# Optimization experiments

Hardware: AMD Instinct MI355X
Metric: run time of the kernel (lower is better)

Reference implementation:

```python
import jax, jax.numpy as jnp
import numpy as np

ALPHA = 0.9     # projection strength
EPS = 1e-3      # Lyapunov positive-definite regularizer (lyapunov_eps)
B, D, H = 32768, 512, 64


def setup_inputs() -> dict:
    key = jax.random.key(0)
    ks = jax.random.split(key, 8)
    def w(k, shape, fan_in):
        return jax.random.normal(k, shape, jnp.float32) * (1.0 / fan_in) ** 0.5
    return dict(
        x=jax.random.normal(ks[0], (B, D), jnp.float32),
        # dynamics MLP f(x): D -> 64 -> 64 -> D
        W1=w(ks[1], (D, H), D), b1=jnp.zeros((H,), jnp.float32),
        W2=w(ks[2], (H, H), H), b2=jnp.zeros((H,), jnp.float32),
        W3=w(ks[3], (H, D), H), b3=jnp.zeros((D,), jnp.float32),
        # Lyapunov MLP V(z): D -> 64 -> 64 -> 1 (+ eps*||z||^2)
        V1=w(ks[4], (D, H), D), c1=jnp.zeros((H,), jnp.float32),
        V2=w(ks[5], (H, H), H), c2=jnp.zeros((H,), jnp.float32),
        V3=w(ks[6], (H, 1), H), c3=jnp.zeros((1,), jnp.float32),
    )


def reference(x, W1, b1, W2, b2, W3, b3, V1, c1, V2, c2, V3, c3):
    def fnet(xx):  # nominal dynamics: [B,D] -> [B,D]
        h = jax.nn.relu(xx @ W1 + b1)
        h = jax.nn.relu(h @ W2 + b2)
        return h @ W3 + b3

    def vnet(z):  # Lyapunov candidate: [B,D] -> [B]
        h = jax.nn.relu(z @ V1 + c1)
        h = jax.nn.relu(h @ V2 + c2)
        return (h @ V3 + c3)[..., 0] + EPS * jnp.sum(z * z, axis=-1)

    def lyap_sum(xx):
        v = vnet(fnet(xx))
        return jnp.sum(v), v

    # grad_v replicates the in-forward lyapunov.backward(...): dV(f(x))/dx, shape [B,D]
    (_, lyap), grad_v = jax.value_and_grad(lyap_sum, has_aux=True)(x)

    f = fnet(x)                                   # [B, D]
    dot = jnp.sum(grad_v * grad_v, axis=-1)       # bmm(gv, fv): per-sample <grad_v, grad_v>
    denom = jnp.sum(grad_v * grad_v)              # global .pow(2).sum() over all elements
    orth = jax.nn.relu(dot + ALPHA * lyap) / denom  # [B]
    return f - orth[:, None] * grad_v             # diag_embed(orth) @ grad_v
```

## Files before the change

### kernel.cpp

```cpp
#include <hip/hip_runtime.h>

#define ALPHA_C 0.9f
#define EPS_C 1e-3f

typedef unsigned short u16;
typedef __attribute__((ext_vector_type(8))) short short8;
typedef __attribute__((ext_vector_type(4))) float f32x4;
#define MFMA(a, b, c) __builtin_amdgcn_mfma_f32_16x16x32_bf16(a, b, c, 0, 0, 0)

__device__ __forceinline__ u16 f2bf(float f) {
  union { float f; unsigned u; } v; v.f = f;
  unsigned u = v.u;
  u += 0x7FFFu + ((u >> 16) & 1u);
  return (u16)(u >> 16);
}
__device__ __forceinline__ float bf2f(u16 h) {
  union { unsigned u; float f; } v; v.u = ((unsigned)h) << 16;
  return v.f;
}

__global__ __launch_bounds__(256) void k_conv(
    const float* __restrict__ W1, const float* __restrict__ W2, const float* __restrict__ W3,
    const float* __restrict__ V1, const float* __restrict__ V2,
    u16* __restrict__ W1T, u16* __restrict__ W1n, u16* __restrict__ W2T, u16* __restrict__ W2n,
    u16* __restrict__ W3T, u16* __restrict__ W3n, u16* __restrict__ V1T, u16* __restrict__ V1n,
    u16* __restrict__ V2T, u16* __restrict__ V2n) {
  int i = blockIdx.x * 256 + threadIdx.x;
  { float v = W1[i]; int k = i >> 6, j = i & 63; u16 b = f2bf(v); W1n[i] = b; W1T[j * 512 + k] = b; }
  { float v = V1[i]; int k = i >> 6, j = i & 63; u16 b = f2bf(v); V1n[i] = b; V1T[j * 512 + k] = b; }
  { float v = W3[i]; int k = i >> 9, n = i & 511; u16 b = f2bf(v); W3n[i] = b; W3T[n * 64 + k] = b; }
  if (i < 4096) {
    { float v = W2[i]; int k = i >> 6, j = i & 63; u16 b = f2bf(v); W2n[i] = b; W2T[j * 64 + k] = b; }
    { float v = V2[i]; int k = i >> 6, j = i & 63; u16 b = f2bf(v); V2n[i] = b; V2T[j * 64 + k] = b; }
  }
}

__global__ __launch_bounds__(256) void k_h12(
    const float* __restrict__ x, const u16* __restrict__ W1T, const float* __restrict__ b1,
    const u16* __restrict__ W2T, const float* __restrict__ b2,
    u16* __restrict__ H1b, u16* __restrict__ H2b) {
  __shared__ u16 As[64 * 136];
  __shared__ u16 Bs[64 * 136];
  __shared__ u16 W2s[64 * 72];
  __shared__ u16 Hs[64 * 72];
  const int tid = threadIdx.x;
  const int lane = tid & 63, w = tid >> 6, q = lane >> 4, r = lane & 15;
  const int m0 = blockIdx.x * 64;

  #pragma unroll
  for (int c = 0; c < 2; ++c) {
    int idx = c * 256 + tid; int a = idx >> 3, k8 = (idx & 7) * 8;
    *(short8*)&W2s[a * 72 + k8] = *(const short8*)&W2T[a * 64 + k8];
  }

  f32x4 acc[4] = {};
  for (int kc = 0; kc < 4; ++kc) {
    __syncthreads();
    #pragma unroll
    for (int c = 0; c < 8; ++c) {
      int idx = c * 256 + tid; int rr = idx >> 5, k4 = (idx & 31) * 4;
      float4 v = *(const float4*)&x[(size_t)(m0 + rr) * 512 + kc * 128 + k4];
      As[rr * 136 + k4 + 0] = f2bf(v.x);
      As[rr * 136 + k4 + 1] = f2bf(v.y);
      As[rr * 136 + k4 + 2] = f2bf(v.z);
      As[rr * 136 + k4 + 3] = f2bf(v.w);
    }
    #pragma unroll
    for (int c = 0; c < 4; ++c) {
      int idx = c * 256 + tid; int rr = idx >> 4, k8 = (idx & 15) * 8;
      *(short8*)&Bs[rr * 136 + k8] = *(const short8*)&W1T[rr * 512 + kc * 128 + k8];
    }
    __syncthreads();
    #pragma unroll
    for (int ks = 0; ks < 4; ++ks) {
      short8 a = *(const short8*)&As[(w * 16 + r) * 136 + ks * 32 + q * 8];
      #pragma unroll
      for (int t = 0; t < 4; ++t) {
        short8 b = *(const short8*)&Bs[(t * 16 + r) * 136 + ks * 32 + q * 8];
        acc[t] = MFMA(a, b, acc[t]);
      }
    }
  }
  __syncthreads();
  #pragma unroll
  for (int t = 0; t < 4; ++t) {
    int col = t * 16 + r; float bv = b1[col];
    #pragma unroll
    for (int g = 0; g < 4; ++g) {
      float h = acc[t][g] + bv; h = h > 0.f ? h : 0.f;
      Hs[(w * 16 + q * 4 + g) * 72 + col] = f2bf(h);
    }
  }
  __syncthreads();
  #pragma unroll
  for (int c = 0; c < 2; ++c) {
    int idx = c * 256 + tid; int rr = idx >> 3, k8 = (idx & 7) * 8;
    *(short8*)&H1b[(size_t)(m0 + rr) * 64 + k8] = *(const short8*)&Hs[rr * 72 + k8];
  }
  f32x4 acc2[4] = {};
  #pragma unroll
  for (int ks = 0; ks < 2; ++ks) {
    short8 a = *(const short8*)&Hs[(w * 16 + r) * 72 + ks * 32 + q * 8];
    #pragma unroll
    for (int t = 0; t < 4; ++t) {
      short8 b = *(const short8*)&W2s[(t * 16 + r) * 72 + ks * 32 + q * 8];
      acc2[t] = MFMA(a, b, acc2[t]);
    }
  }
  __syncthreads();
  #pragma unroll
  for (int t = 0; t < 4; ++t) {
    int col = t * 16 + r; float bv = b2[col];
    #pragma unroll
    for (int g = 0; g < 4; ++g) {
      float h = acc2[t][g] + bv; h = h > 0.f ? h : 0.f;
      Hs[(w * 16 + q * 4 + g) * 72 + col] = f2bf(h);
    }
  }
  __syncthreads();
  #pragma unroll
  for (int c = 0; c < 2; ++c) {
    int idx = c * 256 + tid; int rr = idx >> 3, k8 = (idx & 7) * 8;
    *(short8*)&H2b[(size_t)(m0 + rr) * 64 + k8] = *(const short8*)&Hs[rr * 72 + k8];
  }
}

__global__ __launch_bounds__(256) void k_fg1s(
    const u16* __restrict__ H2b, const u16* __restrict__ W3T, const float* __restrict__ b3,
    const u16* __restrict__ V1T, const float* __restrict__ c1,
    const u16* __restrict__ V2Tb, const u16* __restrict__ V2nb, const float* __restrict__ c2,
    const float* __restrict__ V3, const float* __restrict__ c3,
    u16* __restrict__ Fb, u16* __restrict__ S2b, float* __restrict__ LYAP) {
  __shared__ u16 H2s[64 * 72];
  __shared__ u16 Bs[128 * 72];
  __shared__ u16 As[64 * 136];
  const int tid = threadIdx.x;
  const int lane = tid & 63, w = tid >> 6, q = lane >> 4, r = lane & 15;
  const int m0 = blockIdx.x * 64;

  #pragma unroll
  for (int c = 0; c < 2; ++c) {
    int idx = c * 256 + tid; int a = idx >> 3, k8 = (idx & 7) * 8;
    *(short8*)&H2s[a * 72 + k8] = *(const short8*)&H2b[(size_t)(m0 + a) * 64 + k8];
  }
  f32x4 g1acc[4] = {};
  float ssq[4] = {0.f, 0.f, 0.f, 0.f};
  for (int nc = 0; nc < 4; ++nc) {
    __syncthreads();
    #pragma unroll
    for (int c = 0; c < 4; ++c) {
      int idx = c * 256 + tid; int nl = idx >> 3, k8 = (idx & 7) * 8;
      *(short8*)&Bs[nl * 72 + k8] = *(const short8*)&W3T[(size_t)(nc * 128 + nl) * 64 + k8];
    }
    __syncthreads();
    f32x4 facc[8] = {};
    #pragma unroll
    for (int ks = 0; ks < 2; ++ks) {
      short8 a = *(const short8*)&H2s[(w * 16 + r) * 72 + ks * 32 + q * 8];
      #pragma unroll
      for (int t = 0; t < 8; ++t) {
        short8 b = *(const short8*)&Bs[(t * 16 + r) * 72 + ks * 32 + q * 8];
        facc[t] = MFMA(a, b, facc[t]);
      }
    }
    #pragma unroll
    for (int t = 0; t < 8; ++t) {
      int colg = nc * 128 + t * 16 + r;
      float bv = b3[colg];
      #pragma unroll
      for (int g = 0; g < 4; ++g) {
        float v = facc[t][g] + bv;
        ssq[g] += v * v;
        As[(w * 16 + q * 4 + g) * 136 + t * 16 + r] = f2bf(v);
      }
    }
    __syncthreads();
    #pragma unroll
    for (int c = 0; c < 4; ++c) {
      int idx = c * 256 + tid; int jj = idx >> 4, k8 = (idx & 15) * 8;
      *(short8*)&Bs[jj * 136 + k8] = *(const short8*)&V1T[(size_t)jj * 512 + nc * 128 + k8];
    }
    __syncthreads();
    #pragma unroll
    for (int ks = 0; ks < 4; ++ks) {
      short8 a = *(const short8*)&As[(w * 16 + r) * 136 + ks * 32 + q * 8];
      #pragma unroll
      for (int t = 0; t < 4; ++t) {
        short8 b = *(const short8*)&Bs[(t * 16 + r) * 136 + ks * 32 + q * 8];
        g1acc[t] = MFMA(a, b, g1acc[t]);
      }
    }
    #pragma unroll
    for (int c = 0; c < 4; ++c) {
      int idx = c * 256 + tid; int rr = idx >> 4, k8 = (idx & 15) * 8;
      *(short8*)&Fb[(size_t)(m0 + rr) * 512 + nc * 128 + k8] = *(const short8*)&As[rr * 136 + k8];
    }
  }
  __syncthreads();
  f32x4 g1v[4];
  #pragma unroll
  for (int t = 0; t < 4; ++t) {
    int col = t * 16 + r; float cv = c1[col];
    #pragma unroll
    for (int g = 0; g < 4; ++g) {
      float v = g1acc[t][g] + cv; v = v > 0.f ? v : 0.f;
      g1v[t][g] = v;
      H2s[(w * 16 + q * 4 + g) * 72 + col] = f2bf(v);
    }
  }
  #pragma unroll
  for (int c = 0; c < 2; ++c) {
    int idx = c * 256 + tid; int a = idx >> 3, k8 = (idx & 7) * 8;
    *(short8*)&Bs[a * 72 + k8] = *(const short8*)&V2Tb[a * 64 + k8];
  }
  __syncthreads();
  f32x4 g2acc[4] = {};
  #pragma unroll
  for (int ks = 0; ks < 2; ++ks) {
    short8 a = *(const short8*)&H2s[(w * 16 + r) * 72 + ks * 32 + q * 8];
    #pragma unroll
    for (int t = 0; t < 4; ++t) {
      short8 b = *(const short8*)&Bs[(t * 16 + r) * 72 + ks * 32 + q * 8];
      g2acc[t] = MFMA(a, b, g2acc[t]);
    }
  }
  __syncthreads();
  float tot[4] = {0.f, 0.f, 0.f, 0.f};
  #pragma unroll
  for (int t = 0; t < 4; ++t) {
    int col = t * 16 + r;
    float c2v = c2[col], v3v = V3[col];
    #pragma unroll
    for (int g = 0; g < 4; ++g) {
      float pre = g2acc[t][g] + c2v;
      float g2 = pre > 0.f ? pre : 0.f;
      float s3 = pre > 0.f ? v3v : 0.f;
      H2s[(w * 16 + q * 4 + g) * 72 + col] = f2bf(s3);
      tot[g] += g2 * v3v;
    }
  }
  #pragma unroll
  for (int c = 0; c < 2; ++c) {
    int idx = c * 256 + tid; int a = idx >> 3, k8 = (idx & 7) * 8;
    *(short8*)&Bs[a * 72 + k8] = *(const short8*)&V2nb[a * 64 + k8];
  }
  __syncthreads();
  f32x4 s2acc[4] = {};
  #pragma unroll
  for (int ks = 0; ks < 2; ++ks) {
    short8 a = *(const short8*)&H2s[(w * 16 + r) * 72 + ks * 32 + q * 8];
    #pragma unroll
    for (int t = 0; t < 4; ++t) {
      short8 b = *(const short8*)&Bs[(t * 16 + r) * 72 + ks * 32 + q * 8];
      s2acc[t] = MFMA(a, b, s2acc[t]);
    }
  }
  #pragma unroll
  for (int t = 0; t < 4; ++t) {
    int col = t * 16 + r;
    #pragma unroll
    for (int g = 0; g < 4; ++g) {
      float sv = g1v[t][g] > 0.f ? s2acc[t][g] : 0.f;
      S2b[(size_t)(m0 + w * 16 + q * 4 + g) * 64 + col] = f2bf(sv);
    }
  }
  float c3v = c3[0];
  #pragma unroll
  for (int g = 0; g < 4; ++g) {
    float s = tot[g] + EPS_C * ssq[g];
    s += __shfl_xor(s, 1); s += __shfl_xor(s, 2); s += __shfl_xor(s, 4); s += __shfl_xor(s, 8);
    if (r == 0) LYAP[m0 + w * 16 + q * 4 + g] = s + c3v;
  }
}

__global__ __launch_bounds__(256) void k_utg(
    const u16* __restrict__ S2b, const u16* __restrict__ V1n, const u16* __restrict__ Fb,
    const u16* __restrict__ W3n, const u16* __restrict__ W2n, const u16* __restrict__ W1n,
    const u16* __restrict__ H1b, const u16* __restrict__ H2b,
    const float* __restrict__ LYAP,
    u16* __restrict__ T2b, float* __restrict__ NUM, float* __restrict__ DP) {
  __shared__ u16 S2s[64 * 72];
  __shared__ u16 Bs[128 * 72];
  __shared__ u16 As[64 * 136];
  __shared__ u16 W2s[64 * 72];
  __shared__ u16 T3s[64 * 72];
  __shared__ float dred[4];
  const int tid = threadIdx.x;
  const int lane = tid & 63, w = tid >> 6, q = lane >> 4, r = lane & 15;
  const int m0 = blockIdx.x * 64;

  #pragma unroll
  for (int c = 0; c < 2; ++c) {
    int idx = c * 256 + tid; int a = idx >> 3, k8 = (idx & 7) * 8;
    *(short8*)&S2s[a * 72 + k8] = *(const short8*)&S2b[(size_t)(m0 + a) * 64 + k8];
    *(short8*)&W2s[a * 72 + k8] = *(const short8*)&W2n[a * 64 + k8];
  }
  f32x4 t3acc[4] = {};
  for (int nc = 0; nc < 4; ++nc) {
    __syncthreads();
    #pragma unroll
    for (int c = 0; c < 4; ++c) {
      int idx = c * 256 + tid; int rr = idx >> 4, k8 = (idx & 15) * 8;
      *(short8*)&As[rr * 136 + k8] = *(const short8*)&Fb[(size_t)(m0 + rr) * 512 + nc * 128 + k8];
    }
    #pragma unroll
    for (int c = 0; c < 4; ++c) {
      int idx = c * 256 + tid; int nl = idx >> 3, k8 = (idx & 7) * 8;
      *(short8*)&Bs[nl * 72 + k8] = *(const short8*)&V1n[(size_t)(nc * 128 + nl) * 64 + k8];
    }
    __syncthreads();
    f32x4 uacc[8] = {};
    #pragma unroll
    for (int ks = 0; ks < 2; ++ks) {
      short8 a = *(const short8*)&S2s[(w * 16 + r) * 72 + ks * 32 + q * 8];
      #pragma unroll
      for (int t = 0; t < 8; ++t) {
        short8 b = *(const short8*)&Bs[(t * 16 + r) * 72 + ks * 32 + q * 8];
        uacc[t] = MFMA(a, b, uacc[t]);
      }
    }
    #pragma unroll
    for (int t = 0; t < 8; ++t) {
      #pragma unroll
      for (int g = 0; g < 4; ++g) {
        int addr = (w * 16 + q * 4 + g) * 136 + t * 16 + r;
        As[addr] = f2bf(uacc[t][g] + 2.f * EPS_C * bf2f(As[addr]));
      }
    }
    __syncthreads();
    #pragma unroll
    for (int c = 0; c < 4; ++c) {
      int idx = c * 256 + tid; int jj = idx >> 4, k8 = (idx & 15) * 8;
      *(short8*)&Bs[jj * 136 + k8] = *(const short8*)&W3n[(size_t)jj * 512 + nc * 128 + k8];
    }
    __syncthreads();
    #pragma unroll
    for (int ks = 0; ks < 4; ++ks) {
      short8 a = *(const short8*)&As[(w * 16 + r) * 136 + ks * 32 + q * 8];
      #pragma unroll
      for (int t = 0; t < 4; ++t) {
        short8 b = *(const short8*)&Bs[(t * 16 + r) * 136 + ks * 32 + q * 8];
        t3acc[t] = MFMA(a, b, t3acc[t]);
      }
    }
  }
  #pragma unroll
  for (int t = 0; t < 4; ++t) {
    int col = t * 16 + r;
    #pragma unroll
    for (int g = 0; g < 4; ++g) {
      int rl = w * 16 + q * 4 + g;
      u16 h2u = H2b[(size_t)(m0 + rl) * 64 + col];
      float v = h2u ? t3acc[t][g] : 0.f;
      T3s[rl * 72 + col] = f2bf(v);
    }
  }
  f32x4 t2acc[4] = {};
  #pragma unroll
  for (int ks = 0; ks < 2; ++ks) {
    short8 a = *(const short8*)&T3s[(w * 16 + r) * 72 + ks * 32 + q * 8];
    #pragma unroll
    for (int t = 0; t < 4; ++t) {
      short8 b = *(const short8*)&W2s[(t * 16 + r) * 72 + ks * 32 + q * 8];
      t2acc[t] = MFMA(a, b, t2acc[t]);
    }
  }
  __syncthreads();
  #pragma unroll
  for (int t = 0; t < 4; ++t) {
    int col = t * 16 + r;
    #pragma unroll
    for (int g = 0; g < 4; ++g) {
      int rl = w * 16 + q * 4 + g;
      u16 h1u = H1b[(size_t)(m0 + rl) * 64 + col];
      u16 tv = h1u ? f2bf(t2acc[t][g]) : 0;
      T2b[(size_t)(m0 + rl) * 64 + col] = tv;
      S2s[rl * 72 + col] = tv;
    }
  }
  float ssq[4] = {0.f, 0.f, 0.f, 0.f};
  for (int nc = 0; nc < 4; ++nc) {
    __syncthreads();
    #pragma unroll
    for (int c = 0; c < 4; ++c) {
      int idx = c * 256 + tid; int nl = idx >> 3, k8 = (idx & 7) * 8;
      *(short8*)&Bs[nl * 72 + k8] = *(const short8*)&W1n[(size_t)(nc * 128 + nl) * 64 + k8];
    }
    __syncthreads();
    f32x4 acc[8] = {};
    #pragma unroll
    for (int ks = 0; ks < 2; ++ks) {
      short8 a = *(const short8*)&S2s[(w * 16 + r) * 72 + ks * 32 + q * 8];
      #pragma unroll
      for (int t = 0; t < 8; ++t) {
        short8 b = *(const short8*)&Bs[(t * 16 + r) * 72 + ks * 32 + q * 8];
        acc[t] = MFMA(a, b, acc[t]);
      }
    }
    #pragma unroll
    for (int t = 0; t < 8; ++t)
      #pragma unroll
      for (int g = 0; g < 4; ++g) ssq[g] += acc[t][g] * acc[t][g];
  }
  float totw = 0.f;
  #pragma unroll
  for (int g = 0; g < 4; ++g) {
    float s = ssq[g];
    s += __shfl_xor(s, 1); s += __shfl_xor(s, 2); s += __shfl_xor(s, 4); s += __shfl_xor(s, 8);
    if (r == 0) {
      int rowg = m0 + w * 16 + q * 4 + g;
      float nm = s + ALPHA_C * LYAP[rowg];
      NUM[rowg] = nm > 0.f ? nm : 0.f;
    }
    s += __shfl_xor(s, 16); s += __shfl_xor(s, 32);
    totw += s;
  }
  if (lane == 0) dred[w] = totw;
  __syncthreads();
  if (tid == 0) atomicAdd(&DP[blockIdx.x & 255], dred[0] + dred[1] + dred[2] + dred[3]);
}

__global__ __launch_bounds__(256) void k_out(
    const u16* __restrict__ T2b, const u16* __restrict__ W1n,
    const u16* __restrict__ Fb, const float* __restrict__ NUM, const float* __restrict__ DP,
    float* __restrict__ out) {
  __shared__ u16 T2s[64 * 72];
  __shared__ u16 Bs[128 * 72];
  __shared__ u16 As[64 * 136];
  __shared__ float red[256];
  const int tid = threadIdx.x;
  const int lane = tid & 63, w = tid >> 6, q = lane >> 4, r = lane & 15;
  const int m0 = blockIdx.x * 64;
  red[tid] = DP[tid];
  #pragma unroll
  for (int c = 0; c < 2; ++c) {
    int idx = c * 256 + tid; int a = idx >> 3, k8 = (idx & 7) * 8;
    *(short8*)&T2s[a * 72 + k8] = *(const short8*)&T2b[(size_t)(m0 + a) * 64 + k8];
  }
  __syncthreads();
  for (int s = 128; s >= 1; s >>= 1) {
    if (tid < s) red[tid] += red[tid + s];
    __syncthreads();
  }
  const float inv_denom = 1.f / red[0];
  float sc[4];
  #pragma unroll
  for (int g = 0; g < 4; ++g) sc[g] = NUM[m0 + w * 16 + q * 4 + g] * inv_denom;
  for (int nc = 0; nc < 4; ++nc) {
    __syncthreads();
    #pragma unroll
    for (int c = 0; c < 4; ++c) {
      int idx = c * 256 + tid; int nl = idx >> 3, k8 = (idx & 7) * 8;
      *(short8*)&Bs[nl * 72 + k8] = *(const short8*)&W1n[(size_t)(nc * 128 + nl) * 64 + k8];
    }
    #pragma unroll
    for (int c = 0; c < 4; ++c) {
      int idx = c * 256 + tid; int rr = idx >> 4, k8 = (idx & 15) * 8;
      *(short8*)&As[rr * 136 + k8] = *(const short8*)&Fb[(size_t)(m0 + rr) * 512 + nc * 128 + k8];
    }
    __syncthreads();
    f32x4 acc[8] = {};
    #pragma unroll
    for (int ks = 0; ks < 2; ++ks) {
      short8 a = *(const short8*)&T2s[(w * 16 + r) * 72 + ks * 32 + q * 8];
      #pragma unroll
      for (int t = 0; t < 8; ++t) {
        short8 b = *(const short8*)&Bs[(t * 16 + r) * 72 + ks * 32 + q * 8];
        acc[t] = MFMA(a, b, acc[t]);
      }
    }
    #pragma unroll
    for (int t = 0; t < 8; ++t) {
      int colg = nc * 128 + t * 16 + r;
      #pragma unroll
      for (int g = 0; g < 4; ++g) {
        int rl = w * 16 + q * 4 + g;
        float fv = bf2f(As[rl * 136 + t * 16 + r]);
        out[(size_t)(m0 + rl) * 512 + colg] = fv - sc[g] * acc[t][g];
      }
    }
  }
}

extern "C" void kernel_launch(void* const* d_in, const int* in_sizes, int n_in,
                              void* d_out, int out_size, void* d_ws, size_t ws_size,
                              hipStream_t stream) {
  const float* x  = (const float*)d_in[0];
  const float* W1 = (const float*)d_in[1];
  const float* b1 = (const float*)d_in[2];
  const float* W2 = (const float*)d_in[3];
  const float* b2 = (const float*)d_in[4];
  const float* W3 = (const float*)d_in[5];
  const float* b3 = (const float*)d_in[6];
  const float* V1 = (const float*)d_in[7];
  const float* c1 = (const float*)d_in[8];
  const float* V2 = (const float*)d_in[9];
  const float* c2 = (const float*)d_in[10];
  const float* V3 = (const float*)d_in[11];
  const float* c3 = (const float*)d_in[12];
  float* out = (float*)d_out;

  u16* Fb = (u16*)d_ws;
  float* LYAP = (float*)(Fb + 16777216);
  float* NUM  = LYAP + 32768;
  float* DP   = NUM + 32768;
  u16* H1b  = (u16*)(DP + 256);
  u16* H2b  = H1b + 2097152;
  u16* S2b  = H2b + 2097152;
  u16* T2b  = S2b + 2097152;
  u16* W1Tb = T2b + 2097152;
  u16* W1nb = W1Tb + 32768;
  u16* W2Tb = W1nb + 32768;
  u16* W2nb = W2Tb + 4096;
  u16* W3Tb = W2nb + 4096;
  u16* W3nb = W3Tb + 32768;
  u16* V1Tb = W3nb + 32768;
  u16* V1nb = V1Tb + 32768;
  u16* V2Tb = V1nb + 32768;
  u16* V2nb = V2Tb + 4096;

  hipMemsetAsync(DP, 0, 256 * sizeof(float), stream);

  k_conv<<<128, 256, 0, stream>>>(W1, W2, W3, V1, V2,
                                  W1Tb, W1nb, W2Tb, W2nb, W3Tb, W3nb, V1Tb, V1nb, V2Tb, V2nb);
  k_h12<<<512, 256, 0, stream>>>(x, W1Tb, b1, W2Tb, b2, H1b, H2b);
  k_fg1s<<<512, 256, 0, stream>>>(H2b, W3Tb, b3, V1Tb, c1, V2Tb, V2nb, c2, V3, c3, Fb, S2b, LYAP);
  k_utg<<<512, 256, 0, stream>>>(S2b, V1nb, Fb, W3nb, W2nb, W1nb, H1b, H2b, LYAP, T2b, NUM, DP);
  k_out<<<512, 256, 0, stream>>>(T2b, W1nb, Fb, NUM, DP, out);
}
```

Baseline: 204.1 us.

## Fuse forward hidden layers into F/V kernel, shrink shared memory, simplify denominator reduction

```diff
diff --git a/kernel.cpp b/kernel.cpp
--- a/kernel.cpp
+++ b/kernel.cpp
@@ -1,4 +1,5 @@
 #include <hip/hip_runtime.h>
+#include <hip/hip_bf16.h>
 
 #define ALPHA_C 0.9f
 #define EPS_C 1e-3f
@@ -17,6 +18,10 @@
 __device__ __forceinline__ float bf2f(u16 h) {
   union { unsigned u; float f; } v; v.u = ((unsigned)h) << 16;
   return v.f;
+}
+__device__ __forceinline__ unsigned pkbf(float a, float b) {
+  __hip_bfloat162 t = __float22bfloat162_rn(float2{a, b});
+  union { __hip_bfloat162 h; unsigned u; } cv; cv.h = t; return cv.u;
 }
 
 __global__ __launch_bounds__(256) void k_conv(
@@ -35,24 +40,23 @@
   }
 }
 
-__global__ __launch_bounds__(256) void k_h12(
-    const float* __restrict__ x, const u16* __restrict__ W1T, const float* __restrict__ b1,
+__global__ __launch_bounds__(256) void k_fwd(
+    const float* __restrict__ x,
+    const u16* __restrict__ W1T, const float* __restrict__ b1,
     const u16* __restrict__ W2T, const float* __restrict__ b2,
-    u16* __restrict__ H1b, u16* __restrict__ H2b) {
+    const u16* __restrict__ W3T, const float* __restrict__ b3,
+    const u16* __restrict__ V1T, const float* __restrict__ c1,
+    const u16* __restrict__ V2Tb, const u16* __restrict__ V2nb, const float* __restrict__ c2,
+    const float* __restrict__ V3, const float* __restrict__ c3,
+    u16* __restrict__ H1b, u16* __restrict__ H2b,
+    u16* __restrict__ Fb, u16* __restrict__ S2b, float* __restrict__ LYAP) {
   __shared__ u16 As[64 * 136];
-  __shared__ u16 Bs[64 * 136];
-  __shared__ u16 W2s[64 * 72];
-  __shared__ u16 Hs[64 * 72];
+  __shared__ u16 Bs[128 * 72];
+  __shared__ u16 Cs[64 * 72];
   const int tid = threadIdx.x;
   const int lane = tid & 63, w = tid >> 6, q = lane >> 4, r = lane & 15;
   const int m0 = blockIdx.x * 64;
 
-  #pragma unroll
-  for (int c = 0; c < 2; ++c) {
-    int idx = c * 256 + tid; int a = idx >> 3, k8 = (idx & 7) * 8;
-    *(short8*)&W2s[a * 72 + k8] = *(const short8*)&W2T[a * 64 + k8];
-  }
-
   f32x4 acc[4] = {};
   for (int kc = 0; kc < 4; ++kc) {
     __syncthreads();
@@ -60,10 +64,8 @@
     for (int c = 0; c < 8; ++c) {
       int idx = c * 256 + tid; int rr = idx >> 5, k4 = (idx & 31) * 4;
       float4 v = *(const float4*)&x[(size_t)(m0 + rr) * 512 + kc * 128 + k4];
-      As[rr * 136 + k4 + 0] = f2bf(v.x);
-      As[rr * 136 + k4 + 1] = f2bf(v.y);
-      As[rr * 136 + k4 + 2] = f2bf(v.z);
-      As[rr * 136 + k4 + 3] = f2bf(v.w);
+      uint2 pv; pv.x = pkbf(v.x, v.y); pv.y = pkbf(v.z, v.w);
+      *(uint2*)&As[rr * 136 + k4] = pv;
     }
     #pragma unroll
     for (int c = 0; c < 4; ++c) {
@@ -81,67 +83,47 @@
       }
     }
   }
-  __syncthreads();
   #pragma unroll
   for (int t = 0; t < 4; ++t) {
     int col = t * 16 + r; float bv = b1[col];
     #pragma unroll
     for (int g = 0; g < 4; ++g) {
       float h = acc[t][g] + bv; h = h > 0.f ? h : 0.f;
-      Hs[(w * 16 + q * 4 + g) * 72 + col] = f2bf(h);
-    }
-  }
-  __syncthreads();
-  #pragma unroll
-  for (int c = 0; c < 2; ++c) {
-    int idx = c * 256 + tid; int rr = idx >> 3, k8 = (idx & 7) * 8;
-    *(short8*)&H1b[(size_t)(m0 + rr) * 64 + k8] = *(const short8*)&Hs[rr * 72 + k8];
-  }
+      Cs[(w * 16 + q * 4 + g) * 72 + col] = f2bf(h);
+    }
+  }
+  __syncthreads();
+  #pragma unroll
+  for (int c = 0; c < 2; ++c) {
+    int idx = c * 256 + tid; int a = idx >> 3, k8 = (idx & 7) * 8;
+    *(short8*)&Bs[a * 72 + k8] = *(const short8*)&W2T[a * 64 + k8];
+    *(short8*)&H1b[(size_t)(m0 + a) * 64 + k8] = *(const short8*)&Cs[a * 72 + k8];
+  }
+  __syncthreads();
   f32x4 acc2[4] = {};
   #pragma unroll
   for (int ks = 0; ks < 2; ++ks) {
-    short8 a = *(const short8*)&Hs[(w * 16 + r) * 72 + ks * 32 + q * 8];
+    short8 a = *(const short8*)&Cs[(w * 16 + r) * 72 + ks * 32 + q * 8];
     #pragma unroll
     for (int t = 0; t < 4; ++t) {
-      short8 b = *(const short8*)&W2s[(t * 16 + r) * 72 + ks * 32 + q * 8];
+      short8 b = *(const short8*)&Bs[(t * 16 + r) * 72 + ks * 32 + q * 8];
       acc2[t] = MFMA(a, b, acc2[t]);
     }
   }
-  __syncthreads();
   #pragma unroll
   for (int t = 0; t < 4; ++t) {
     int col = t * 16 + r; float bv = b2[col];
     #pragma unroll
     for (int g = 0; g < 4; ++g) {
       float h = acc2[t][g] + bv; h = h > 0.f ? h : 0.f;
-      Hs[(w * 16 + q * 4 + g) * 72 + col] = f2bf(h);
-    }
-  }
-  __syncthreads();
-  #pragma unroll
-  for (int c = 0; c < 2; ++c) {
-    int idx = c * 256 + tid; int rr = idx >> 3, k8 = (idx & 7) * 8;
-    *(short8*)&H2b[(size_t)(m0 + rr) * 64 + k8] = *(const short8*)&Hs[rr * 72 + k8];
-  }
-}
-
-__global__ __launch_bounds__(256) void k_fg1s(
-    const u16* __restrict__ H2b, const u16* __restrict__ W3T, const float* __restrict__ b3,
-    const u16* __restrict__ V1T, const float* __restrict__ c1,
-    const u16* __restrict__ V2Tb, const u16* __restrict__ V2nb, const float* __restrict__ c2,
-    const float* __restrict__ V3, const float* __restrict__ c3,
-    u16* __restrict__ Fb, u16* __restrict__ S2b, float* __restrict__ LYAP) {
-  __shared__ u16 H2s[64 * 72];
-  __shared__ u16 Bs[128 * 72];
-  __shared__ u16 As[64 * 136];
-  const int tid = threadIdx.x;
-  const int lane = tid & 63, w = tid >> 6, q = lane >> 4, r = lane & 15;
-  const int m0 = blockIdx.x * 64;
-
-  #pragma unroll
-  for (int c = 0; c < 2; ++c) {
-    int idx = c * 256 + tid; int a = idx >> 3, k8 = (idx & 7) * 8;
-    *(short8*)&H2s[a * 72 + k8] = *(const short8*)&H2b[(size_t)(m0 + a) * 64 + k8];
+      Cs[(w * 16 + q * 4 + g) * 72 + col] = f2bf(h);
+    }
+  }
+  __syncthreads();
+  #pragma unroll
+  for (int c = 0; c < 2; ++c) {
+    int idx = c * 256 + tid; int a = idx >> 3, k8 = (idx & 7) * 8;
+    *(short8*)&H2b[(size_t)(m0 + a) * 64 + k8] = *(const short8*)&Cs[a * 72 + k8];
   }
   f32x4 g1acc[4] = {};
   float ssq[4] = {0.f, 0.f, 0.f, 0.f};
@@ -156,7 +138,7 @@
     f32x4 facc[8] = {};
     #pragma unroll
     for (int ks = 0; ks < 2; ++ks) {
-      short8 a = *(const short8*)&H2s[(w * 16 + r) * 72 + ks * 32 + q * 8];
+      short8 a = *(const short8*)&Cs[(w * 16 + r) * 72 + ks * 32 + q * 8];
       #pragma unroll
       for (int t = 0; t < 8; ++t) {
         short8 b = *(const short8*)&Bs[(t * 16 + r) * 72 + ks * 32 + q * 8];
@@ -205,7 +187,7 @@
     for (int g = 0; g < 4; ++g) {
       float v = g1acc[t][g] + cv; v = v > 0.f ? v : 0.f;
       g1v[t][g] = v;
-      H2s[(w * 16 + q * 4 + g) * 72 + col] = f2bf(v);
+      Cs[(w * 16 + q * 4 + g) * 72 + col] = f2bf(v);
     }
   }
   #pragma unroll
@@ -217,7 +199,7 @@
   f32x4 g2acc[4] = {};
   #pragma unroll
   for (int ks = 0; ks < 2; ++ks) {
-    short8 a = *(const short8*)&H2s[(w * 16 + r) * 72 + ks * 32 + q * 8];
+    short8 a = *(const short8*)&Cs[(w * 16 + r) * 72 + ks * 32 + q * 8];
     #pragma unroll
     for (int t = 0; t < 4; ++t) {
       short8 b = *(const short8*)&Bs[(t * 16 + r) * 72 + ks * 32 + q * 8];
@@ -235,7 +217,7 @@
       float pre = g2acc[t][g] + c2v;
       float g2 = pre > 0.f ? pre : 0.f;
       float s3 = pre > 0.f ? v3v : 0.f;
-      H2s[(w * 16 + q * 4 + g) * 72 + col] = f2bf(s3);
+      Cs[(w * 16 + q * 4 + g) * 72 + col] = f2bf(s3);
       tot[g] += g2 * v3v;
     }
   }
@@ -248,7 +230,7 @@
   f32x4 s2acc[4] = {};
   #pragma unroll
   for (int ks = 0; ks < 2; ++ks) {
-    short8 a = *(const short8*)&H2s[(w * 16 + r) * 72 + ks * 32 + q * 8];
+    short8 a = *(const short8*)&Cs[(w * 16 + r) * 72 + ks * 32 + q * 8];
     #pragma unroll
     for (int t = 0; t < 4; ++t) {
       short8 b = *(const short8*)&Bs[(t * 16 + r) * 72 + ks * 32 + q * 8];
@@ -279,12 +261,9 @@
     const u16* __restrict__ H1b, const u16* __restrict__ H2b,
     const float* __restrict__ LYAP,
     u16* __restrict__ T2b, float* __restrict__ NUM, float* __restrict__ DP) {
-  __shared__ u16 S2s[64 * 72];
+  __shared__ u16 As[64 * 136];
   __shared__ u16 Bs[128 * 72];
-  __shared__ u16 As[64 * 136];
-  __shared__ u16 W2s[64 * 72];
-  __shared__ u16 T3s[64 * 72];
-  __shared__ float dred[4];
+  __shared__ u16 Cs[64 * 72];
   const int tid = threadIdx.x;
   const int lane = tid & 63, w = tid >> 6, q = lane >> 4, r = lane & 15;
   const int m0 = blockIdx.x * 64;
@@ -292,8 +271,7 @@
   #pragma unroll
   for (int c = 0; c < 2; ++c) {
     int idx = c * 256 + tid; int a = idx >> 3, k8 = (idx & 7) * 8;
-    *(short8*)&S2s[a * 72 + k8] = *(const short8*)&S2b[(size_t)(m0 + a) * 64 + k8];
-    *(short8*)&W2s[a * 72 + k8] = *(const short8*)&W2n[a * 64 + k8];
+    *(short8*)&Cs[a * 72 + k8] = *(const short8*)&S2b[(size_t)(m0 + a) * 64 + k8];
   }
   f32x4 t3acc[4] = {};
   for (int nc = 0; nc < 4; ++nc) {
@@ -312,7 +290,7 @@
     f32x4 uacc[8] = {};
     #pragma unroll
     for (int ks = 0; ks < 2; ++ks) {
-      short8 a = *(const short8*)&S2s[(w * 16 + r) * 72 + ks * 32 + q * 8];
+      short8 a = *(const short8*)&Cs[(w * 16 + r) * 72 + ks * 32 + q * 8];
       #pragma unroll
       for (int t = 0; t < 8; ++t) {
         short8 b = *(const short8*)&Bs[(t * 16 + r) * 72 + ks * 32 + q * 8];
@@ -344,6 +322,12 @@
       }
     }
   }
+  __syncthreads();
+  #pragma unroll
+  for (int c = 0; c < 2; ++c) {
+    int idx = c * 256 + tid; int a = idx >> 3, k8 = (idx & 7) * 8;
+    *(short8*)&Bs[a * 72 + k8] = *(const short8*)&W2n[a * 64 + k8];
+  }
   #pragma unroll
   for (int t = 0; t < 4; ++t) {
     int col = t * 16 + r;
@@ -351,21 +335,20 @@
     for (int g = 0; g < 4; ++g) {
       int rl = w * 16 + q * 4 + g;
       u16 h2u = H2b[(size_t)(m0 + rl) * 64 + col];
-      float v = h2u ? t3acc[t][g] : 0.f;
-      T3s[rl * 72 + col] = f2bf(v);
-    }
-  }
+      Cs[rl * 72 + col] = h2u ? f2bf(t3acc[t][g]) : 0;
+    }
+  }
+  __syncthreads();
   f32x4 t2acc[4] = {};
   #pragma unroll
   for (int ks = 0; ks < 2; ++ks) {
-    short8 a = *(const short8*)&T3s[(w * 16 + r) * 72 + ks * 32 + q * 8];
+    short8 a = *(const short8*)&Cs[(w * 16 + r) * 72 + ks * 32 + q * 8];
     #pragma unroll
     for (int t = 0; t < 4; ++t) {
-      short8 b = *(const short8*)&W2s[(t * 16 + r) * 72 + ks * 32 + q * 8];
+      short8 b = *(const short8*)&Bs[(t * 16 + r) * 72 + ks * 32 + q * 8];
       t2acc[t] = MFMA(a, b, t2acc[t]);
     }
   }
-  __syncthreads();
   #pragma unroll
   for (int t = 0; t < 4; ++t) {
     int col = t * 16 + r;
@@ -375,7 +358,7 @@
       u16 h1u = H1b[(size_t)(m0 + rl) * 64 + col];
       u16 tv = h1u ? f2bf(t2acc[t][g]) : 0;
       T2b[(size_t)(m0 + rl) * 64 + col] = tv;
-      S2s[rl * 72 + col] = tv;
+      Cs[rl * 72 + col] = tv;
     }
   }
   float ssq[4] = {0.f, 0.f, 0.f, 0.f};
@@ -390,7 +373,7 @@
     f32x4 acc[8] = {};
     #pragma unroll
     for (int ks = 0; ks < 2; ++ks) {
-      short8 a = *(const short8*)&S2s[(w * 16 + r) * 72 + ks * 32 + q * 8];
+      short8 a = *(const short8*)&Cs[(w * 16 + r) * 72 + ks * 32 + q * 8];
       #pragma unroll
       for (int t = 0; t < 8; ++t) {
         short8 b = *(const short8*)&Bs[(t * 16 + r) * 72 + ks * 32 + q * 8];
@@ -415,34 +398,25 @@
     s += __shfl_xor(s, 16); s += __shfl_xor(s, 32);
     totw += s;
   }
-  if (lane == 0) dred[w] = totw;
-  __syncthreads();
-  if (tid == 0) atomicAdd(&DP[blockIdx.x & 255], dred[0] + dred[1] + dred[2] + dred[3]);
+  if (lane == 0) atomicAdd(&DP[0], totw);
 }
 
 __global__ __launch_bounds__(256) void k_out(
     const u16* __restrict__ T2b, const u16* __restrict__ W1n,
     const u16* __restrict__ Fb, const float* __restrict__ NUM, const float* __restrict__ DP,
     float* __restrict__ out) {
-  __shared__ u16 T2s[64 * 72];
+  __shared__ u16 As[64 * 136];
   __shared__ u16 Bs[128 * 72];
-  __shared__ u16 As[64 * 136];
-  __shared__ float red[256];
+  __shared__ u16 Cs[64 * 72];
   const int tid = threadIdx.x;
   const int lane = tid & 63, w = tid >> 6, q = lane >> 4, r = lane & 15;
   const int m0 = blockIdx.x * 64;
-  red[tid] = DP[tid];
-  #pragma unroll
-  for (int c = 0; c < 2; ++c) {
-    int idx = c * 256 + tid; int a = idx >> 3, k8 = (idx & 7) * 8;
-    *(short8*)&T2s[a * 72 + k8] = *(const short8*)&T2b[(size_t)(m0 + a) * 64 + k8];
-  }
-  __syncthreads();
-  for (int s = 128; s >= 1; s >>= 1) {
-    if (tid < s) red[tid] += red[tid + s];
-    __syncthreads();
-  }
-  const float inv_denom = 1.f / red[0];
+  #pragma unroll
+  for (int c = 0; c < 2; ++c) {
+    int idx = c * 256 + tid; int a = idx >> 3, k8 = (idx & 7) * 8;
+    *(short8*)&Cs[a * 72 + k8] = *(const short8*)&T2b[(size_t)(m0 + a) * 64 + k8];
+  }
+  const float inv_denom = 1.f / DP[0];
   float sc[4];
   #pragma unroll
   for (int g = 0; g < 4; ++g) sc[g] = NUM[m0 + w * 16 + q * 4 + g] * inv_denom;
@@ -462,7 +436,7 @@
     f32x4 acc[8] = {};
     #pragma unroll
     for (int ks = 0; ks < 2; ++ks) {
-      short8 a = *(const short8*)&T2s[(w * 16 + r) * 72 + ks * 32 + q * 8];
+      short8 a = *(const short8*)&Cs[(w * 16 + r) * 72 + ks * 32 + q * 8];
       #pragma unroll
       for (int t = 0; t < 8; ++t) {
         short8 b = *(const short8*)&Bs[(t * 16 + r) * 72 + ks * 32 + q * 8];
@@ -523,8 +497,8 @@
 
   k_conv<<<128, 256, 0, stream>>>(W1, W2, W3, V1, V2,
                                   W1Tb, W1nb, W2Tb, W2nb, W3Tb, W3nb, V1Tb, V1nb, V2Tb, V2nb);
-  k_h12<<<512, 256, 0, stream>>>(x, W1Tb, b1, W2Tb, b2, H1b, H2b);
-  k_fg1s<<<512, 256, 0, stream>>>(H2b, W3Tb, b3, V1Tb, c1, V2Tb, V2nb, c2, V3, c3, Fb, S2b, LYAP);
+  k_fwd<<<512, 256, 0, stream>>>(x, W1Tb, b1, W2Tb, b2, W3Tb, b3, V1Tb, c1,
+                                 V2Tb, V2nb, c2, V3, c3, H1b, H2b, Fb, S2b, LYAP);
   k_utg<<<512, 256, 0, stream>>>(S2b, V1nb, Fb, W3nb, W2nb, W1nb, H1b, H2b, LYAP, T2b, NUM, DP);
   k_out<<<512, 256, 0, stream>>>(T2b, W1nb, Fb, NUM, DP, out);
 }
```

Measured after the change: 233.8 us. +14.5%, slower.
